# Optimization experiments

Measured on AMD Instinct MI355X. Metric: run time of the kernel, lower is better.

The kernel has to match this reference:

```python
import jax, jax.numpy as jnp
import numpy as np

M = 768   # num edges
N = 768   # num loops (== M because original tiles image_x with len(edge_x) for both)
C = 256
IMG = 1024
CAT = 3 * C + IMG  # 1792, 'sharing' suffix without '1d'/'noimage'
EPS = 1e-4


def _lin_block(x, W, b):
    # LinearBlock: Linear + ReLU
    return jax.nn.relu(x @ W + b)


def _pred_head(x, W1, b1, W2, b2):
    # Sequential(LinearBlock(256,64), Linear(64,1)) -> sigmoid -> flatten
    return jax.nn.sigmoid(_lin_block(x, W1, b1) @ W2 + b2).reshape(-1)


def setup_inputs() -> dict:
    key = jax.random.key(0)
    ks = jax.random.split(key, 24)
    s = 0.02
    return {
        "edge_x": jax.random.normal(ks[0], (M, C), jnp.float32),
        "loop_x": jax.random.normal(ks[1], (N, C), jnp.float32),
        "image_x": jax.random.normal(ks[2], (1, IMG), jnp.float32),
        "loop_edge_masks": (jax.random.uniform(ks[3], (N, M)) < 0.3).astype(jnp.float32),
        "edge_conflict_mask": (jax.random.uniform(ks[4], (M, M)) < 0.1).astype(jnp.float32),
        "loop_conflict_mask": (jax.random.uniform(ks[5], (N, N)) < 0.1).astype(jnp.float32),
        "loop_masks": jax.random.uniform(ks[6], (N, 64), jnp.float32),      # pass-through only
        "loop_edge_indices": jax.random.randint(ks[7], (N,), 0, M, jnp.int32),  # unused ('1d' off)
        "edge_info": jax.random.normal(ks[8], (M, 4), jnp.float32),         # unused ('1d' off)
        "W_e3": jax.random.normal(ks[9], (CAT, C), jnp.float32) * s,
        "b_e3": jnp.zeros((C,), jnp.float32),
        "W_l3": jax.random.normal(ks[10], (CAT, C), jnp.float32) * s,
        "b_l3": jnp.zeros((C,), jnp.float32),
        "W_ep1": jax.random.normal(ks[11], (C, 64), jnp.float32) * s,
        "b_ep1": jnp.zeros((64,), jnp.float32),
        "W_ep2": jax.random.normal(ks[12], (64, 1), jnp.float32) * s,
        "b_ep2": jnp.zeros((1,), jnp.float32),
        "W_lp1": jax.random.normal(ks[13], (C, 64), jnp.float32) * s,
        "b_lp1": jnp.zeros((64,), jnp.float32),
        "W_lp2": jax.random.normal(ks[14], (64, 1), jnp.float32) * s,
        "b_lp2": jnp.zeros((1,), jnp.float32),
    }


def reference(edge_x, loop_x, image_x, loop_edge_masks, edge_conflict_mask,
              loop_conflict_mask, loop_masks, loop_edge_indices, edge_info,
              W_e3, b_e3, W_l3, b_l3, W_ep1, b_ep1, W_ep2, b_ep2,
              W_lp1, b_lp1, W_lp2, b_lp2):
    # iteration-0 predictions (appended to results in original)
    e0 = _pred_head(edge_x, W_ep1, b_ep1, W_ep2, b_ep2)  # [M]
    l0 = _pred_head(loop_x, W_lp1, b_lp1, W_lp2, b_lp2)  # [N]

    # weights[n, m] = mask * |loop_pred[n] - edge_pred[m]|
    w = loop_edge_masks * jnp.abs(l0[:, None] - e0[None, :])  # [N, M]

    # weighted broadcast sums (einsum == unsqueeze-multiply-sum in the original)
    edge_x_from_loop = jnp.einsum('nm,nc->mc', w, loop_x) \
        / jnp.maximum(w.sum(0), EPS)[:, None]               # [M, C]
    loop_x_from_edge = jnp.einsum('nm,mc->nc', w, edge_x) \
        / jnp.maximum(w.sum(1), EPS)[:, None]               # [N, C]

    # conflict-masked max pooling (materializes [M,M,C]/[N,N,C] like the original)
    edge_x_from_conflict = jnp.max(edge_conflict_mask[:, :, None] * edge_x[None, :, :], axis=1)
    loop_x_from_conflict = jnp.max(loop_conflict_mask[:, :, None] * loop_x[None, :, :], axis=1)

    img_e = jnp.broadcast_to(image_x, (edge_x.shape[0], image_x.shape[1]))
    img_l = jnp.broadcast_to(image_x, (loop_x.shape[0], image_x.shape[1]))

    edge_x2 = _lin_block(jnp.concatenate([edge_x, edge_x_from_loop, edge_x_from_conflict, img_e], axis=-1), W_e3, b_e3)
    loop_x2 = _lin_block(jnp.concatenate([loop_x, loop_x_from_edge, loop_x_from_conflict, img_l], axis=-1), W_l3, b_l3)

    e1 = _pred_head(edge_x2, W_ep1, b_ep1, W_ep2, b_ep2)
    l1 = _pred_head(loop_x2, W_lp1, b_lp1, W_lp2, b_lp2)

    # original returns results=[[e0,l0,masks,loop_masks],[e1,l1,masks,loop_masks]];
    # masks are constant pass-throughs, so we return the predictions concatenated.
    return jnp.concatenate([e0, l0, e1, l1])  # [2*(M+N)] = [3072]
```

## Files before the change

kernel.cpp:

```cpp
#include <hip/hip_runtime.h>
#include <hip/hip_bf16.h>
#include <math.h>

#define MM 768
#define CC 256
#define EPSV 1e-4f

__device__ __forceinline__ float sigmoidf_(float x) { return 1.0f / (1.0f + expf(-x)); }

__global__ __launch_bounds__(256) void k_prep(
    const float* __restrict__ edge_x, const float* __restrict__ loop_x,
    const float* __restrict__ image_x,
    const float* __restrict__ ecm, const float* __restrict__ lcm,
    const float* __restrict__ We3, const float* __restrict__ Wl3,
    const float* __restrict__ Wep1, const float* __restrict__ bep1,
    const float* __restrict__ Wep2, const float* __restrict__ bep2,
    const float* __restrict__ Wlp1, const float* __restrict__ blp1,
    const float* __restrict__ Wlp2, const float* __restrict__ blp2,
    float* __restrict__ out, float* __restrict__ efc, float* __restrict__ lfc,
    float* __restrict__ imgpart)
{
    int bid = blockIdx.x;
    int t   = threadIdx.x;

    if (bid < 1536) {
        __shared__ int   s_cnt;
        __shared__ int   s_idx[MM];
        __shared__ float s_val[MM];
        bool isLoop = bid >= MM;
        int  m      = bid & (MM - 1);
        const float* mask = isLoop ? lcm : ecm;
        const float* x    = isLoop ? loop_x : edge_x;
        float*       o    = isLoop ? lfc : efc;

        if (t == 0) s_cnt = 0;
        __syncthreads();
        #pragma unroll
        for (int r = 0; r < 3; ++r) {
            int j = t + r * 256;
            float v = mask[m * MM + j];
            if (v != 0.0f) {
                int p = atomicAdd(&s_cnt, 1);
                s_idx[p] = j;
                s_val[p] = v;
            }
        }
        __syncthreads();
        int cnt = s_cnt;
        float acc = (cnt < MM) ? 0.0f : -INFINITY;
        #pragma unroll 4
        for (int i = 0; i < cnt; ++i)
            acc = fmaxf(acc, s_val[i] * x[s_idx[i] * CC + t]);
        o[m * CC + t] = acc;

    } else if (bid < 1920) {
        int wave = t >> 6, lane = t & 63;
        int row  = (bid - 1536) * 4 + wave;
        const float *x, *W1, *b1, *W2;
        float b2v;
        if (row < MM) { x = edge_x + row * CC;        W1 = Wep1; b1 = bep1; W2 = Wep2; b2v = bep2[0]; }
        else          { x = loop_x + (row - MM) * CC; W1 = Wlp1; b1 = blp1; W2 = Wlp2; b2v = blp2[0]; }

        float a0 = 0.f, a1 = 0.f, a2 = 0.f, a3 = 0.f;
        for (int cc = 0; cc < CC; cc += 4) {
            float4 xv = *reinterpret_cast<const float4*>(x + cc);
            a0 = fmaf(xv.x, W1[(cc + 0) * 64 + lane], a0);
            a1 = fmaf(xv.y, W1[(cc + 1) * 64 + lane], a1);
            a2 = fmaf(xv.z, W1[(cc + 2) * 64 + lane], a2);
            a3 = fmaf(xv.w, W1[(cc + 3) * 64 + lane], a3);
        }
        float h = fmaxf(b1[lane] + ((a0 + a1) + (a2 + a3)), 0.0f);
        float p = h * W2[lane];
        #pragma unroll
        for (int off = 32; off; off >>= 1) p += __shfl_xor(p, off, 64);
        if (lane == 0) out[row] = sigmoidf_(p + b2v);

    } else {
        int sub   = bid - 1920;
        int chunk = sub & 3;
        int head  = sub >> 2;
        const float* W = head ? Wl3 : We3;
        int k0 = chunk * 256;
        float s = 0.0f;
        #pragma unroll 4
        for (int k = 0; k < 256; ++k)
            s = fmaf(image_x[k0 + k], W[(768 + k0 + k) * CC + t], s);
        imgpart[head * 1024 + chunk * 256 + t] = s;
    }
}

__global__ __launch_bounds__(512) void k_bsum(
    const float* __restrict__ lem, const float* __restrict__ edge_x,
    const float* __restrict__ loop_x, const float* __restrict__ pred,
    float* __restrict__ efl, float* __restrict__ lfe)
{
    __shared__ float4 s_wv4[1536];
    __shared__ float  s_ps[512];
    __shared__ float  s_sum[8];
    float* s_wv = reinterpret_cast<float*>(s_wv4);

    int bid = blockIdx.x;
    int t   = threadIdx.x;
    const float* e0 = pred;
    const float* l0 = pred + MM;

    bool isE = bid < 96;
    int  r0  = (isE ? bid : bid - 96) * 8;
    const float* ownp = isE ? e0 : l0;
    const float* othp = isE ? l0 : e0;

    float own[8];
    #pragma unroll
    for (int i = 0; i < 8; ++i) own[i] = ownp[r0 + i];

    #pragma unroll
    for (int k = 0; k < 12; ++k) {
        int idx = t + k * 512;
        int s = idx >> 3, i = idx & 7;
        float lm = isE ? lem[s * MM + r0 + i] : lem[(r0 + i) * MM + s];
        s_wv[idx] = lm * fabsf(othp[s] - own[i]);
    }
    __syncthreads();

    {
        int g = t >> 3, i = t & 7;
        float s = 0.f;
        #pragma unroll
        for (int j = 0; j < 12; ++j) s += s_wv[(g + 64 * j) * 8 + i];
        s_ps[g * 8 + i] = s;
    }
    __syncthreads();
    if (t < 8) {
        float s = 0.f;
        for (int g = 0; g < 64; ++g) s += s_ps[g * 8 + t];
        s_sum[t] = fmaxf(s, EPSV);
    }

    const float* xsrc = isE ? loop_x : edge_x;
    int c = t & 255, h = t >> 8;
    float acc[8] = {0.f, 0.f, 0.f, 0.f, 0.f, 0.f, 0.f, 0.f};
    int s0 = h * 384;
    #pragma unroll 2
    for (int s = s0; s < s0 + 384; ++s) {
        float4 w0 = *reinterpret_cast<const float4*>(&s_wv[s * 8]);
        float4 w1 = *reinterpret_cast<const float4*>(&s_wv[s * 8 + 4]);
        float xv = xsrc[s * CC + c];
        acc[0] = fmaf(w0.x, xv, acc[0]);
        acc[1] = fmaf(w0.y, xv, acc[1]);
        acc[2] = fmaf(w0.z, xv, acc[2]);
        acc[3] = fmaf(w0.w, xv, acc[3]);
        acc[4] = fmaf(w1.x, xv, acc[4]);
        acc[5] = fmaf(w1.y, xv, acc[5]);
        acc[6] = fmaf(w1.z, xv, acc[6]);
        acc[7] = fmaf(w1.w, xv, acc[7]);
    }
    __syncthreads();
    if (h == 1) {
        #pragma unroll
        for (int i = 0; i < 8; ++i) s_wv[i * CC + c] = acc[i];
    }
    __syncthreads();
    if (h == 0) {
        float* outp = isE ? efl : lfe;
        #pragma unroll
        for (int i = 0; i < 8; ++i)
            outp[(r0 + i) * CC + c] = (acc[i] + s_wv[i * CC + c]) / s_sum[i];
    }
}

__global__ __launch_bounds__(512) void k_cat(
    const float* __restrict__ edge_x, const float* __restrict__ loop_x,
    const float* __restrict__ efl, const float* __restrict__ lfe,
    const float* __restrict__ efc, const float* __restrict__ lfc,
    const float* __restrict__ We3, const float* __restrict__ be3,
    const float* __restrict__ Wl3, const float* __restrict__ bl3,
    const float* __restrict__ imgpart,
    const float* __restrict__ Wep1, const float* __restrict__ bep1,
    const float* __restrict__ Wep2, const float* __restrict__ bep2,
    const float* __restrict__ Wlp1, const float* __restrict__ blp1,
    const float* __restrict__ Wlp2, const float* __restrict__ blp2,
    float* __restrict__ out)
{
    __shared__ float4 s_act4[8 * 64];
    float* s_act = reinterpret_cast<float*>(s_act4);

    int head = blockIdx.y;
    const float* W  = head ? Wl3 : We3;
    const float* b  = head ? bl3 : be3;
    const float* x0 = head ? loop_x : edge_x;
    const float* x1 = head ? lfe : efl;
    const float* x2 = head ? lfc : efc;
    const float* ip = imgpart + head * 1024;

    int m0 = blockIdx.x * 8;
    int t  = threadIdx.x;
    int c  = t & 255, h = t >> 8;

    float acc[8] = {0.f, 0.f, 0.f, 0.f, 0.f, 0.f, 0.f, 0.f};

    auto accum = [&](const float* src, int ks, int kw, int len) {
        for (int kk = 0; kk < len; kk += 4) {
            float4 xv[8];
            #pragma unroll
            for (int i = 0; i < 8; ++i)
                xv[i] = *reinterpret_cast<const float4*>(src + (m0 + i) * CC + ks + kk);
            #pragma unroll
            for (int j = 0; j < 4; ++j) {
                float wv = W[(kw + kk + j) * CC + c];
                #pragma unroll
                for (int i = 0; i < 8; ++i)
                    acc[i] = fmaf(reinterpret_cast<const float*>(&xv[i])[j], wv, acc[i]);
            }
        }
    };
    if (h == 0) { accum(x0, 0, 0, 256);   accum(x1, 0, 256, 128); }
    else        { accum(x1, 128, 384, 128); accum(x2, 0, 512, 256); }

    if (h == 1) {
        #pragma unroll
        for (int i = 0; i < 8; ++i) s_act[i * CC + c] = acc[i];
    }
    __syncthreads();
    if (h == 0) {
        float bias = b[c] + ip[c] + ip[256 + c] + ip[512 + c] + ip[768 + c];
        #pragma unroll
        for (int i = 0; i < 8; ++i)
            s_act[i * CC + c] = fmaxf(bias + acc[i] + s_act[i * CC + c], 0.0f);
    }
    __syncthreads();

    int wave = t >> 6, lane = t & 63;
    const float* W1 = head ? Wlp1 : Wep1;
    const float* b1 = head ? blp1 : bep1;
    const float* W2 = head ? Wlp2 : Wep2;
    float b2v       = head ? blp2[0] : bep2[0];
    const float* xr = s_act + wave * CC;

    float a0 = 0.f, a1 = 0.f, a2 = 0.f, a3 = 0.f;
    for (int cc = 0; cc < CC; cc += 4) {
        float4 xv = *reinterpret_cast<const float4*>(xr + cc);
        a0 = fmaf(xv.x, W1[(cc + 0) * 64 + lane], a0);
        a1 = fmaf(xv.y, W1[(cc + 1) * 64 + lane], a1);
        a2 = fmaf(xv.z, W1[(cc + 2) * 64 + lane], a2);
        a3 = fmaf(xv.w, W1[(cc + 3) * 64 + lane], a3);
    }
    float hh = fmaxf(b1[lane] + ((a0 + a1) + (a2 + a3)), 0.0f);
    float p = hh * W2[lane];
    #pragma unroll
    for (int off = 32; off; off >>= 1) p += __shfl_xor(p, off, 64);
    if (lane == 0) out[1536 + head * MM + m0 + wave] = sigmoidf_(p + b2v);
}

extern "C" void kernel_launch(void* const* d_in, const int* in_sizes, int n_in,
                              void* d_out, int out_size, void* d_ws, size_t ws_size,
                              hipStream_t stream)
{
    const float* edge_x  = (const float*)d_in[0];
    const float* loop_x  = (const float*)d_in[1];
    const float* image_x = (const float*)d_in[2];
    const float* lem     = (const float*)d_in[3];
    const float* ecm     = (const float*)d_in[4];
    const float* lcm     = (const float*)d_in[5];
    const float* We3  = (const float*)d_in[9];
    const float* be3  = (const float*)d_in[10];
    const float* Wl3  = (const float*)d_in[11];
    const float* bl3  = (const float*)d_in[12];
    const float* Wep1 = (const float*)d_in[13];
    const float* bep1 = (const float*)d_in[14];
    const float* Wep2 = (const float*)d_in[15];
    const float* bep2 = (const float*)d_in[16];
    const float* Wlp1 = (const float*)d_in[17];
    const float* blp1 = (const float*)d_in[18];
    const float* Wlp2 = (const float*)d_in[19];
    const float* blp2 = (const float*)d_in[20];

    float* out = (float*)d_out;
    float* ws  = (float*)d_ws;

    float* imgpart = ws;
    float* efl     = ws + 2048;
    float* lfe     = efl + MM * CC;
    float* efc     = lfe + MM * CC;
    float* lfc     = efc + MM * CC;

    k_prep<<<1928, 256, 0, stream>>>(edge_x, loop_x, image_x, ecm, lcm,
                                     We3, Wl3,
                                     Wep1, bep1, Wep2, bep2,
                                     Wlp1, blp1, Wlp2, blp2,
                                     out, efc, lfc, imgpart);

    k_bsum<<<192, 512, 0, stream>>>(lem, edge_x, loop_x, out, efl, lfe);

    k_cat<<<dim3(96, 2), 512, 0, stream>>>(edge_x, loop_x, efl, lfe, efc, lfc,
                                           We3, be3, Wl3, bl3, imgpart,
                                           Wep1, bep1, Wep2, bep2,
                                           Wlp1, blp1, Wlp2, blp2, out);
}
```

Measured before the change: 194.8 us.

## Halve rows per block in bsum/cat, ballot-compact masks, split pred-head K

k_prep now compacts the conflict-mask nonzeros with a wave ballot and prefix popcount instead of per-element shared atomics, and splits the max-pool loop into four independent accumulators. k_bsum and k_cat process 4 rows per block instead of 8, doubling the grid to 384 blocks each for better occupancy on the many CUs. k_bsum computes its row sums with wave shuffles instead of a two-stage shared reduction. k_cat splits the prediction-head dot product across two waves per row, which adds an extra barrier. The trade-off is that weight rows are reloaded by twice as many blocks.

```diff
diff --git a/kernel.cpp b/kernel.cpp
--- a/kernel.cpp
+++ b/kernel.cpp
@@ -35,23 +35,34 @@
 
         if (t == 0) s_cnt = 0;
         __syncthreads();
+        int lane = t & 63;
         #pragma unroll
         for (int r = 0; r < 3; ++r) {
             int j = t + r * 256;
             float v = mask[m * MM + j];
-            if (v != 0.0f) {
-                int p = atomicAdd(&s_cnt, 1);
-                s_idx[p] = j;
-                s_val[p] = v;
-            }
+            bool nz = (v != 0.0f);
+            unsigned long long b = __ballot(nz);
+            int prefix = __popcll(b & ((1ull << lane) - 1ull));
+            int cntw   = __popcll(b);
+            int base = 0;
+            if (lane == 0 && cntw) base = atomicAdd(&s_cnt, cntw);
+            base = __shfl(base, 0, 64);
+            if (nz) { s_idx[base + prefix] = j; s_val[base + prefix] = v; }
         }
         __syncthreads();
         int cnt = s_cnt;
-        float acc = (cnt < MM) ? 0.0f : -INFINITY;
-        #pragma unroll 4
-        for (int i = 0; i < cnt; ++i)
-            acc = fmaxf(acc, s_val[i] * x[s_idx[i] * CC + t]);
-        o[m * CC + t] = acc;
+        float init = (cnt < MM) ? 0.0f : -INFINITY;
+        float a0 = init, a1 = init, a2 = init, a3 = init;
+        int i = 0;
+        for (; i + 4 <= cnt; i += 4) {
+            a0 = fmaxf(a0, s_val[i + 0] * x[s_idx[i + 0] * CC + t]);
+            a1 = fmaxf(a1, s_val[i + 1] * x[s_idx[i + 1] * CC + t]);
+            a2 = fmaxf(a2, s_val[i + 2] * x[s_idx[i + 2] * CC + t]);
+            a3 = fmaxf(a3, s_val[i + 3] * x[s_idx[i + 3] * CC + t]);
+        }
+        for (; i < cnt; ++i)
+            a0 = fmaxf(a0, s_val[i] * x[s_idx[i] * CC + t]);
+        o[m * CC + t] = fmaxf(fmaxf(a0, a1), fmaxf(a2, a3));
 
     } else if (bid < 1920) {
         int wave = t >> 6, lane = t & 63;
@@ -94,9 +105,9 @@
     const float* __restrict__ loop_x, const float* __restrict__ pred,
     float* __restrict__ efl, float* __restrict__ lfe)
 {
-    __shared__ float4 s_wv4[1536];
-    __shared__ float  s_ps[512];
-    __shared__ float  s_sum[8];
+    __shared__ float4 s_wv4[MM];
+    __shared__ float  s_pw[8 * 4];
+    __shared__ float  s_sum[4];
     float* s_wv = reinterpret_cast<float*>(s_wv4);
 
     int bid = blockIdx.x;
@@ -104,67 +115,76 @@
     const float* e0 = pred;
     const float* l0 = pred + MM;
 
-    bool isE = bid < 96;
-    int  r0  = (isE ? bid : bid - 96) * 8;
+    bool isE = bid < 192;
+    int  r0  = (isE ? bid : bid - 192) * 4;
     const float* ownp = isE ? e0 : l0;
     const float* othp = isE ? l0 : e0;
 
-    float own[8];
+    float own[4];
     #pragma unroll
-    for (int i = 0; i < 8; ++i) own[i] = ownp[r0 + i];
-
+    for (int i = 0; i < 4; ++i) own[i] = ownp[r0 + i];
+
+    int i_ = t & 3;
+    float myown = own[0];
+    if (i_ == 1) myown = own[1];
+    else if (i_ == 2) myown = own[2];
+    else if (i_ == 3) myown = own[3];
+    float psum = 0.f;
     #pragma unroll
-    for (int k = 0; k < 12; ++k) {
+    for (int k = 0; k < 6; ++k) {
         int idx = t + k * 512;
-        int s = idx >> 3, i = idx & 7;
-        float lm = isE ? lem[s * MM + r0 + i] : lem[(r0 + i) * MM + s];
-        s_wv[idx] = lm * fabsf(othp[s] - own[i]);
-    }
-    __syncthreads();
-
-    {
-        int g = t >> 3, i = t & 7;
+        int s = idx >> 2;
+        float lm = isE ? lem[s * MM + r0 + i_] : lem[(r0 + i_) * MM + s];
+        float wv = lm * fabsf(othp[s] - myown);
+        s_wv[idx] = wv;
+        psum += wv;
+    }
+    #pragma unroll
+    for (int off = 4; off < 64; off <<= 1) psum += __shfl_xor(psum, off, 64);
+    int wave = t >> 6, lane = t & 63;
+    if (lane < 4) s_pw[wave * 4 + lane] = psum;
+    __syncthreads();
+    if (t < 4) {
         float s = 0.f;
         #pragma unroll
-        for (int j = 0; j < 12; ++j) s += s_wv[(g + 64 * j) * 8 + i];
-        s_ps[g * 8 + i] = s;
-    }
-    __syncthreads();
-    if (t < 8) {
-        float s = 0.f;
-        for (int g = 0; g < 64; ++g) s += s_ps[g * 8 + t];
+        for (int w = 0; w < 8; ++w) s += s_pw[w * 4 + t];
         s_sum[t] = fmaxf(s, EPSV);
     }
 
     const float* xsrc = isE ? loop_x : edge_x;
     int c = t & 255, h = t >> 8;
-    float acc[8] = {0.f, 0.f, 0.f, 0.f, 0.f, 0.f, 0.f, 0.f};
+    float acc0 = 0.f, acc1 = 0.f, acc2 = 0.f, acc3 = 0.f;
     int s0 = h * 384;
-    #pragma unroll 2
-    for (int s = s0; s < s0 + 384; ++s) {
-        float4 w0 = *reinterpret_cast<const float4*>(&s_wv[s * 8]);
-        float4 w1 = *reinterpret_cast<const float4*>(&s_wv[s * 8 + 4]);
-        float xv = xsrc[s * CC + c];
-        acc[0] = fmaf(w0.x, xv, acc[0]);
-        acc[1] = fmaf(w0.y, xv, acc[1]);
-        acc[2] = fmaf(w0.z, xv, acc[2]);
-        acc[3] = fmaf(w0.w, xv, acc[3]);
-        acc[4] = fmaf(w1.x, xv, acc[4]);
-        acc[5] = fmaf(w1.y, xv, acc[5]);
-        acc[6] = fmaf(w1.z, xv, acc[6]);
-        acc[7] = fmaf(w1.w, xv, acc[7]);
+    for (int s = s0; s < s0 + 384; s += 4) {
+        float4 wa = s_wv4[s + 0];
+        float4 wb = s_wv4[s + 1];
+        float4 wc = s_wv4[s + 2];
+        float4 wd = s_wv4[s + 3];
+        float xa = xsrc[(s + 0) * CC + c];
+        float xb = xsrc[(s + 1) * CC + c];
+        float xc = xsrc[(s + 2) * CC + c];
+        float xd = xsrc[(s + 3) * CC + c];
+        acc0 = fmaf(wa.x, xa, acc0); acc1 = fmaf(wa.y, xa, acc1);
+        acc2 = fmaf(wa.z, xa, acc2); acc3 = fmaf(wa.w, xa, acc3);
+        acc0 = fmaf(wb.x, xb, acc0); acc1 = fmaf(wb.y, xb, acc1);
+        acc2 = fmaf(wb.z, xb, acc2); acc3 = fmaf(wb.w, xb, acc3);
+        acc0 = fmaf(wc.x, xc, acc0); acc1 = fmaf(wc.y, xc, acc1);
+        acc2 = fmaf(wc.z, xc, acc2); acc3 = fmaf(wc.w, xc, acc3);
+        acc0 = fmaf(wd.x, xd, acc0); acc1 = fmaf(wd.y, xd, acc1);
+        acc2 = fmaf(wd.z, xd, acc2); acc3 = fmaf(wd.w, xd, acc3);
     }
     __syncthreads();
     if (h == 1) {
-        #pragma unroll
-        for (int i = 0; i < 8; ++i) s_wv[i * CC + c] = acc[i];
+        s_wv[0 * CC + c] = acc0; s_wv[1 * CC + c] = acc1;
+        s_wv[2 * CC + c] = acc2; s_wv[3 * CC + c] = acc3;
     }
     __syncthreads();
     if (h == 0) {
         float* outp = isE ? efl : lfe;
-        #pragma unroll
-        for (int i = 0; i < 8; ++i)
-            outp[(r0 + i) * CC + c] = (acc[i] + s_wv[i * CC + c]) / s_sum[i];
+        outp[(r0 + 0) * CC + c] = (acc0 + s_wv[0 * CC + c]) / s_sum[0];
+        outp[(r0 + 1) * CC + c] = (acc1 + s_wv[1 * CC + c]) / s_sum[1];
+        outp[(r0 + 2) * CC + c] = (acc2 + s_wv[2 * CC + c]) / s_sum[2];
+        outp[(r0 + 3) * CC + c] = (acc3 + s_wv[3 * CC + c]) / s_sum[3];
     }
 }
 
@@ -181,8 +201,9 @@
     const float* __restrict__ Wlp2, const float* __restrict__ blp2,
     float* __restrict__ out)
 {
-    __shared__ float4 s_act4[8 * 64];
-    float* s_act = reinterpret_cast<float*>(s_act4);
+    __shared__ float s_part[4 * CC];
+    __shared__ float s_act[4 * CC];
+    __shared__ float s_h[8 * 64];
 
     int head = blockIdx.y;
     const float* W  = head ? Wl3 : We3;
@@ -192,63 +213,69 @@
     const float* x2 = head ? lfc : efc;
     const float* ip = imgpart + head * 1024;
 
-    int m0 = blockIdx.x * 8;
+    int m0 = blockIdx.x * 4;
     int t  = threadIdx.x;
     int c  = t & 255, h = t >> 8;
 
-    float acc[8] = {0.f, 0.f, 0.f, 0.f, 0.f, 0.f, 0.f, 0.f};
+    float acc[4] = {0.f, 0.f, 0.f, 0.f};
 
     auto accum = [&](const float* src, int ks, int kw, int len) {
         for (int kk = 0; kk < len; kk += 4) {
-            float4 xv[8];
+            float4 xv[4];
             #pragma unroll
-            for (int i = 0; i < 8; ++i)
+            for (int i = 0; i < 4; ++i)
                 xv[i] = *reinterpret_cast<const float4*>(src + (m0 + i) * CC + ks + kk);
             #pragma unroll
             for (int j = 0; j < 4; ++j) {
                 float wv = W[(kw + kk + j) * CC + c];
                 #pragma unroll
-                for (int i = 0; i < 8; ++i)
+                for (int i = 0; i < 4; ++i)
                     acc[i] = fmaf(reinterpret_cast<const float*>(&xv[i])[j], wv, acc[i]);
             }
         }
     };
-    if (h == 0) { accum(x0, 0, 0, 256);   accum(x1, 0, 256, 128); }
+    if (h == 0) { accum(x0, 0, 0, 256);     accum(x1, 0, 256, 128); }
     else        { accum(x1, 128, 384, 128); accum(x2, 0, 512, 256); }
 
     if (h == 1) {
         #pragma unroll
-        for (int i = 0; i < 8; ++i) s_act[i * CC + c] = acc[i];
+        for (int i = 0; i < 4; ++i) s_part[i * CC + c] = acc[i];
     }
     __syncthreads();
     if (h == 0) {
         float bias = b[c] + ip[c] + ip[256 + c] + ip[512 + c] + ip[768 + c];
         #pragma unroll
-        for (int i = 0; i < 8; ++i)
-            s_act[i * CC + c] = fmaxf(bias + acc[i] + s_act[i * CC + c], 0.0f);
+        for (int i = 0; i < 4; ++i)
+            s_act[i * CC + c] = fmaxf(bias + acc[i] + s_part[i * CC + c], 0.0f);
     }
     __syncthreads();
 
     int wave = t >> 6, lane = t & 63;
+    int row = wave >> 1, khalf = wave & 1;
     const float* W1 = head ? Wlp1 : Wep1;
     const float* b1 = head ? blp1 : bep1;
     const float* W2 = head ? Wlp2 : Wep2;
     float b2v       = head ? blp2[0] : bep2[0];
-    const float* xr = s_act + wave * CC;
+    const float* xr = s_act + row * CC + khalf * 128;
 
     float a0 = 0.f, a1 = 0.f, a2 = 0.f, a3 = 0.f;
-    for (int cc = 0; cc < CC; cc += 4) {
+    for (int cc = 0; cc < 128; cc += 4) {
         float4 xv = *reinterpret_cast<const float4*>(xr + cc);
-        a0 = fmaf(xv.x, W1[(cc + 0) * 64 + lane], a0);
-        a1 = fmaf(xv.y, W1[(cc + 1) * 64 + lane], a1);
-        a2 = fmaf(xv.z, W1[(cc + 2) * 64 + lane], a2);
-        a3 = fmaf(xv.w, W1[(cc + 3) * 64 + lane], a3);
-    }
-    float hh = fmaxf(b1[lane] + ((a0 + a1) + (a2 + a3)), 0.0f);
-    float p = hh * W2[lane];
-    #pragma unroll
-    for (int off = 32; off; off >>= 1) p += __shfl_xor(p, off, 64);
-    if (lane == 0) out[1536 + head * MM + m0 + wave] = sigmoidf_(p + b2v);
+        int kb = khalf * 128 + cc;
+        a0 = fmaf(xv.x, W1[(kb + 0) * 64 + lane], a0);
+        a1 = fmaf(xv.y, W1[(kb + 1) * 64 + lane], a1);
+        a2 = fmaf(xv.z, W1[(kb + 2) * 64 + lane], a2);
+        a3 = fmaf(xv.w, W1[(kb + 3) * 64 + lane], a3);
+    }
+    s_h[wave * 64 + lane] = (a0 + a1) + (a2 + a3);
+    __syncthreads();
+    if (khalf == 0) {
+        float hv = fmaxf(b1[lane] + s_h[wave * 64 + lane] + s_h[(wave + 1) * 64 + lane], 0.0f);
+        float p = hv * W2[lane];
+        #pragma unroll
+        for (int off = 32; off; off >>= 1) p += __shfl_xor(p, off, 64);
+        if (lane == 0) out[1536 + head * MM + m0 + row] = sigmoidf_(p + b2v);
+    }
 }
 
 extern "C" void kernel_launch(void* const* d_in, const int* in_sizes, int n_in,
@@ -289,10 +316,10 @@
                                      Wlp1, blp1, Wlp2, blp2,
                                      out, efc, lfc, imgpart);
 
-    k_bsum<<<192, 512, 0, stream>>>(lem, edge_x, loop_x, out, efl, lfe);
-
-    k_cat<<<dim3(96, 2), 512, 0, stream>>>(edge_x, loop_x, efl, lfe, efc, lfc,
-                                           We3, be3, Wl3, bl3, imgpart,
-                                           Wep1, bep1, Wep2, bep2,
-                                           Wlp1, blp1, Wlp2, blp2, out);
+    k_bsum<<<384, 512, 0, stream>>>(lem, edge_x, loop_x, out, efl, lfe);
+
+    k_cat<<<dim3(192, 2), 512, 0, stream>>>(edge_x, loop_x, efl, lfe, efc, lfc,
+                                            We3, be3, Wl3, bl3, imgpart,
+                                            Wep1, bep1, Wep2, bep2,
+                                            Wlp1, blp1, Wlp2, blp2, out);
 }
```

Measured after the change: 169.9 us. 12.8% less time.
